# Kernel optimization log

Hardware: AMD Instinct MI355X
Metric: run time of the kernel (lower is better)

Reference implementation:

```python
import jax, jax.numpy as jnp
import numpy as np

B, S, D, H, E, K = 2, 2048, 1024, 4096, 8, 2


def setup_inputs() -> dict:
    key = jax.random.key(0)
    ks = jax.random.split(key, 7)
    sd = 1.0 / np.sqrt(D)
    sh = 1.0 / np.sqrt(H)
    return {
        "x": jax.random.normal(ks[0], (B, S, D), dtype=jnp.float32),
        "Wr": jax.random.uniform(ks[1], (D, E), jnp.float32, -sd, sd),
        "br": jnp.zeros((E,), jnp.float32),
        "W1": jax.random.uniform(ks[2], (E, D, H), jnp.float32, -sd, sd),
        "b1": jax.random.uniform(ks[3], (E, H), jnp.float32, -sd, sd),
        "W2": jax.random.uniform(ks[4], (E, H, D), jnp.float32, -sh, sh),
        "b2": jax.random.uniform(ks[5], (E, D), jnp.float32, -sh, sh),
    }


def reference(x, Wr, br, W1, b1, W2, b2):
    # Router
    router_logits = jnp.einsum("bsd,de->bse", x, Wr) + br          # [B,S,E]
    topk_logits, topk_idx = jax.lax.top_k(router_logits, K)          # [B,S,K]
    gates = jax.nn.softmax(topk_logits, axis=-1)                     # [B,S,K]

    # Dense all-expert FFN (math identical to masked per-expert GEMMs)
    h = jax.nn.gelu(jnp.einsum("bsd,edh->ebsh", x, W1) + b1[:, None, None, :],
                    approximate=False)                                # [E,B,S,H]
    y = jnp.einsum("ebsh,ehd->bsed", h, W2) + b2[None, None, :, :]    # [B,S,E,D]

    # Gather the top-k experts per token and combine with gates
    sel = jnp.take_along_axis(y, topk_idx[..., None], axis=2)         # [B,S,K,D]
    out = jnp.sum(gates[..., None] * sel, axis=2)                     # [B,S,D]

    # Load-balancing aux loss
    probs = jax.nn.softmax(router_logits, axis=-1)
    importance = probs.mean(axis=(0, 1))                              # [E]
    aux_loss = jnp.mean((importance - 1.0 / E) ** 2)
    return out, aux_loss
```

## Files before the change

### kernel.cpp

```cpp
#include <hip/hip_runtime.h>
#include <hip/hip_bf16.h>
#include <math.h>

#define NTOK 4096
#define DD   1024
#define HH   4096
#define EE   8
#define NSLOT 8192
#define NSLOT_PAD 8448
#define RBLK 128

typedef __bf16 bf16x8 __attribute__((ext_vector_type(8)));
typedef float  f32x4  __attribute__((ext_vector_type(4)));
typedef unsigned short u16x8 __attribute__((ext_vector_type(8)));

#define WAITCNT_VM(n) (((n) & 0xF) | (0x7 << 4) | (0xF << 8) | (((n) >> 4) << 14))

#define WS_COUNTS     0
#define WS_CURSORS    64
#define WS_OFFSETS    128
#define WS_IMP        256
#define WS_TOPK_IDX   512
#define WS_TOPK_GATE  33280
#define WS_SLOT_OF    66048
#define WS_TOKEN_LIST 98816
#define WS_XG         131584
#define WS_HBUF       17433088
#define WS_YBUF       86639104
#define WS_W1BT       120193536
#define WS_W2BT       187302400
#define WS_CNT_PART   (WS_HBUF + (size_t)NSLOT * HH * 2)
#define WS_IMP_PART   (WS_HBUF + (size_t)NSLOT * HH * 2 + 4096)

__device__ __forceinline__ float gelu_exact(float v) {
    return 0.5f * v * (1.0f + erff(v * 0.70710678118654752f));
}

__device__ __forceinline__ void async_copy16(const __bf16* g, __bf16* l) {
    __builtin_amdgcn_global_load_lds(
        (const __attribute__((address_space(1))) void*)g,
        (__attribute__((address_space(3))) void*)l, 16, 0, 0);
}

__launch_bounds__(256)
__global__ void router_kernel(const float* __restrict__ x,
                              const float* __restrict__ Wr,
                              const float* __restrict__ br,
                              int* __restrict__ cntPart,
                              float* __restrict__ impPart,
                              int* __restrict__ topk_idx,
                              float* __restrict__ topk_gate) {
    __shared__ float WrL[DD * EE];
    __shared__ float impW[4][EE];
    __shared__ int cntL[EE];
    int tid = threadIdx.x;
    int lane = tid & 63, wave = tid >> 6;
    int grp = lane >> 3, e = lane & 7;
    int t = blockIdx.x * 32 + wave * 8 + grp;

    for (int i = tid; i < DD * EE / 4; i += 256)
        ((float4*)WrL)[i] = ((const float4*)Wr)[i];
    if (tid < EE) cntL[tid] = 0;
    __syncthreads();

    const float* xr = x + (size_t)t * DD;
    float acc = 0.f;
#pragma unroll 4
    for (int d = 0; d < DD; d += 4) {
        float4 xv = *(const float4*)(xr + d);
        acc = fmaf(xv.x, WrL[(d + 0) * EE + e], acc);
        acc = fmaf(xv.y, WrL[(d + 1) * EE + e], acc);
        acc = fmaf(xv.z, WrL[(d + 2) * EE + e], acc);
        acc = fmaf(xv.w, WrL[(d + 3) * EE + e], acc);
    }
    float l = acc + br[e];

    float m = l;
#pragma unroll
    for (int mk = 1; mk <= 4; mk <<= 1) m = fmaxf(m, __shfl_xor(m, mk, 64));
    float p = expf(l - m);
    float s = p;
#pragma unroll
    for (int mk = 1; mk <= 4; mk <<= 1) s += __shfl_xor(s, mk, 64);
    p /= s;

    float bl = l; int be = e;
#pragma unroll
    for (int mk = 1; mk <= 4; mk <<= 1) {
        float ol = __shfl_xor(bl, mk, 64);
        int   oe = __shfl_xor(be, mk, 64);
        if (ol > bl || (ol == bl && oe < be)) { bl = ol; be = oe; }
    }
    int e1 = be; float l1 = bl;
    float cl = (e == e1) ? -INFINITY : l; int ce = e;
#pragma unroll
    for (int mk = 1; mk <= 4; mk <<= 1) {
        float ol = __shfl_xor(cl, mk, 64);
        int   oe = __shfl_xor(ce, mk, 64);
        if (ol > cl || (ol == cl && oe < ce)) { cl = ol; ce = oe; }
    }
    int e2 = ce; float l2 = cl;

    if (e == 0) {
        float bb = expf(l2 - l1);
        float g1 = 1.f / (1.f + bb);
        topk_idx[t * 2 + 0] = e1; topk_idx[t * 2 + 1] = e2;
        topk_gate[t * 2 + 0] = g1; topk_gate[t * 2 + 1] = bb * g1;
        atomicAdd(&cntL[e1], 1);
        atomicAdd(&cntL[e2], 1);
    }

#pragma unroll
    for (int mk = 8; mk <= 32; mk <<= 1) p += __shfl_xor(p, mk, 64);
    if (lane < 8) impW[wave][lane] = p;
    __syncthreads();
    if (tid < EE) {
        float v = impW[0][tid] + impW[1][tid] + impW[2][tid] + impW[3][tid];
        impPart[blockIdx.x * EE + tid] = v;
        cntPart[blockIdx.x * EE + tid] = cntL[tid];
    }
}

__launch_bounds__(256)
__global__ void scatter_kernel(const int* __restrict__ topk_idx,
                               const int* __restrict__ cntPart,
                               const float* __restrict__ impPart,
                               int* __restrict__ offsets,
                               int* __restrict__ token_list,
                               int* __restrict__ slot_of,
                               float* __restrict__ aux_out) {
    __shared__ int tot[EE], bef[EE], lcnt[EE];
    __shared__ float impS[EE];
    __shared__ int off[EE + 1];
    int tid = threadIdx.x, b = blockIdx.x;
    if (tid < EE) { tot[tid] = 0; bef[tid] = 0; lcnt[tid] = 0; impS[tid] = 0.f; }
    __syncthreads();
#pragma unroll
    for (int i = 0; i < 4; i++) {
        int idx = tid * 4 + i;
        int rb = idx >> 3, e = idx & 7;
        int c = cntPart[idx];
        atomicAdd(&tot[e], c);
        if (rb < b * 8) atomicAdd(&bef[e], c);
        if (b == 0) atomicAdd(&impS[e], impPart[idx]);
    }
    __syncthreads();
    if (tid == 0) {
        int o = 0;
        for (int e = 0; e < EE; e++) { off[e] = o; o += tot[e]; }
        off[EE] = o;
        if (b == 0) {
            for (int e = 0; e <= EE; e++) offsets[e] = off[e];
            float aux = 0.f;
            for (int e = 0; e < EE; e++) {
                float d = impS[e] / (float)NTOK - 1.0f / (float)EE;
                aux += d * d;
            }
            aux_out[0] = aux / (float)EE;
        }
    }
    __syncthreads();
    int t = b * 256 + tid;
    int e0 = topk_idx[t * 2 + 0], e1 = topk_idx[t * 2 + 1];
    int r0 = atomicAdd(&lcnt[e0], 1);
    int r1 = atomicAdd(&lcnt[e1], 1);
    int s0 = off[e0] + bef[e0] + r0;
    int s1 = off[e1] + bef[e1] + r1;
    token_list[s0] = t; token_list[s1] = t;
    slot_of[t * 2 + 0] = s0; slot_of[t * 2 + 1] = s1;
}

__launch_bounds__(256)
__global__ void gather_x_kernel(const float* __restrict__ x,
                                const int* __restrict__ token_list,
                                __bf16* __restrict__ xg) {
    int s = blockIdx.x;
    int t = token_list[s];
    int tid = threadIdx.x;
    float4 v = ((const float4*)(x + (size_t)t * DD))[tid];
    __bf16 tmp[4] __attribute__((aligned(8)));
    tmp[0] = (__bf16)v.x; tmp[1] = (__bf16)v.y;
    tmp[2] = (__bf16)v.z; tmp[3] = (__bf16)v.w;
    ((ushort4*)(xg + (size_t)s * DD))[tid] = *(ushort4*)tmp;
}

__launch_bounds__(256)
__global__ void transpose_w2_kernel(const float* __restrict__ W1,
                                    const float* __restrict__ W2,
                                    __bf16* __restrict__ W1bt,
                                    __bf16* __restrict__ W2bt) {
    int id = blockIdx.x;
    bool isw2 = id >= 8192;
    int rem = id & 8191;
    int e = rem >> 10, t = rem & 1023;
    const float* in; __bf16* out; int R, C, cx, ry;
    if (!isw2) { in = W1; out = W1bt; R = DD; C = HH; cx = t & 63; ry = t >> 6; }
    else       { in = W2; out = W2bt; R = HH; C = DD; cx = t & 15; ry = t >> 4; }
    int c0 = cx * 64, r0 = ry * 64;
    __shared__ float tile[64][65];
    int tid = threadIdx.x;
    const float* ip = in + (size_t)e * R * C;
#pragma unroll
    for (int i = 0; i < 4; i++) {
        int flat = i * 256 + tid;
        int r = flat >> 4, c4 = (flat & 15) * 4;
        float4 v = *(const float4*)(ip + (size_t)(r0 + r) * C + c0 + c4);
        tile[r][c4 + 0] = v.x; tile[r][c4 + 1] = v.y;
        tile[r][c4 + 2] = v.z; tile[r][c4 + 3] = v.w;
    }
    __syncthreads();
    __bf16* op = out + (size_t)e * C * R;
#pragma unroll
    for (int i = 0; i < 2; i++) {
        int flat = i * 256 + tid;
        int c = flat >> 3, r8 = (flat & 7) * 8;
        __bf16 tmp[8] __attribute__((aligned(16)));
#pragma unroll
        for (int j = 0; j < 8; j++) tmp[j] = (__bf16)tile[r8 + j][c];
        *(u16x8*)(op + (size_t)(c0 + c) * R + r0 + r8) = *(u16x8*)tmp;
    }
}

template <int N, int K, bool GELU, typename OutT>
__launch_bounds__(512, 4)
__global__ void gemm128_kernel(const __bf16* __restrict__ A,
                               const __bf16* __restrict__ Bt,
                               const float* __restrict__ bias,
                               const int* __restrict__ offsets,
                               OutT* __restrict__ Out) {
    constexpr int NT = K / 64;
    int e = blockIdx.z, ct = blockIdx.x, rt = blockIdx.y;
    int obase = offsets[e], cnt = offsets[e + 1] - obase;
    int m0 = rt * 128;
    if (m0 >= cnt) return;

    __shared__ __bf16 As[2][2][8 * 512];
    __shared__ __bf16 Bs[2][16 * 512];

    int tid = threadIdx.x, lane = tid & 63, wave = tid >> 6;
    int quad = lane >> 4, m16 = lane & 15;
    int wm = wave & 3, wn = wave >> 2;
    int srow = lane >> 3;
    int scol = ((lane & 7) ^ srow) * 8;

    const __bf16* Ag = A + (size_t)(obase + m0) * K + scol;
    const __bf16* Bg = Bt + ((size_t)e * N + (size_t)ct * 128) * K + scol;

    const __bf16* pA[2];
    const __bf16* pB[2];
#pragma unroll
    for (int h = 0; h < 2; h++) pA[h] = Ag + (size_t)(h * 64 + wave * 8 + srow) * K;
#pragma unroll
    for (int p = 0; p < 2; p++) pB[p] = Bg + (size_t)(p * 64 + wave * 8 + srow) * K;

    int swz = m16 & 7;
    int abase = (wm * 2 + (m16 >> 3)) * 512 + swz * 64;
    int bbase[4];
#pragma unroll
    for (int ni = 0; ni < 4; ni++)
        bbase[ni] = (ni * 4 + wn * 2 + (m16 >> 3)) * 512 + swz * 64;

    f32x4 acc[2][4] = {};
    bf16x8 af[2], bfr[4][2];

#define STG_A(buf, h, k0) async_copy16(pA[h] + (k0), &As[buf][h][wave * 512]);
#define STG_B(buf, k0)                                                        \
    { async_copy16(pB[0] + (k0), &Bs[buf][wave * 512]);                       \
      async_copy16(pB[1] + (k0), &Bs[buf][(wave + 8) * 512]); }

#define READ_A(buf, h)                                                        \
    { af[0] = *(const bf16x8*)(&As[buf][h][abase] + ((quad ^ swz) * 8));      \
      af[1] = *(const bf16x8*)(&As[buf][h][abase] + (((4 + quad) ^ swz) * 8)); }
#define READ_B(buf)                                                           \
    { _Pragma("unroll")                                                       \
      for (int ni = 0; ni < 4; ni++) {                                        \
          bfr[ni][0] = *(const bf16x8*)(&Bs[buf][bbase[ni]] + ((quad ^ swz) * 8)); \
          bfr[ni][1] = *(const bf16x8*)(&Bs[buf][bbase[ni]] + (((4 + quad) ^ swz) * 8)); } }

#define MMA(h)                                                                \
    { __builtin_amdgcn_s_setprio(1);                                         \
      _Pragma("unroll")                                                       \
      for (int kk = 0; kk < 2; kk++)                                          \
          _Pragma("unroll")                                                   \
          for (int ni = 0; ni < 4; ni++)                                      \
              acc[h][ni] = __builtin_amdgcn_mfma_f32_16x16x32_bf16(           \
                  af[kk], bfr[ni][kk], acc[h][ni], 0, 0, 0);                  \
      __builtin_amdgcn_s_setprio(0); }

    STG_A(0, 0, 0);
    STG_B(0, 0);
    STG_A(0, 1, 0);

    int cur = 0;
    for (int t = 0; t < NT - 1; t++) {
        int k1 = (t + 1) * 64, nxt = cur ^ 1;
        __builtin_amdgcn_s_waitcnt(WAITCNT_VM(1));
        __builtin_amdgcn_s_barrier();
        READ_A(cur, 0); READ_B(cur);
        STG_A(nxt, 0, k1); STG_B(nxt, k1);
        MMA(0);
        __builtin_amdgcn_s_waitcnt(WAITCNT_VM(3));
        __builtin_amdgcn_s_barrier();
        READ_A(cur, 1);
        STG_A(nxt, 1, k1);
        MMA(1);
        cur = nxt;
    }
    __builtin_amdgcn_s_waitcnt(WAITCNT_VM(1));
    __builtin_amdgcn_s_barrier();
    READ_A(cur, 0); READ_B(cur);
    MMA(0);
    __builtin_amdgcn_s_waitcnt(WAITCNT_VM(0));
    __builtin_amdgcn_s_barrier();
    READ_A(cur, 1);
    MMA(1);
#undef STG_A
#undef STG_B
#undef READ_A
#undef READ_B
#undef MMA

    float bv[4];
#pragma unroll
    for (int ni = 0; ni < 4; ni++)
        bv[ni] = bias[(size_t)e * N + ct * 128 + (ni * 2 + wn) * 16 + m16];
#pragma unroll
    for (int mi = 0; mi < 2; mi++) {
#pragma unroll
        for (int rr = 0; rr < 4; rr++) {
            int row = (mi * 4 + wm) * 16 + quad * 4 + rr;
            if (m0 + row < cnt) {
                size_t orow = (size_t)(obase + m0 + row) * N + (size_t)ct * 128;
#pragma unroll
                for (int ni = 0; ni < 4; ni++) {
                    float v = acc[mi][ni][rr] + bv[ni];
                    if (GELU) v = gelu_exact(v);
                    Out[orow + (ni * 2 + wn) * 16 + m16] = (OutT)v;
                }
            }
        }
    }
}

__launch_bounds__(256)
__global__ void combine_kernel(const float* __restrict__ ybuf,
                               const int* __restrict__ slot_of,
                               const float* __restrict__ topk_gate,
                               float* __restrict__ out) {
    int t = blockIdx.x;
    int tid = threadIdx.x;
    int s0 = slot_of[t * 2 + 0], s1 = slot_of[t * 2 + 1];
    float g0 = topk_gate[t * 2 + 0], g1 = topk_gate[t * 2 + 1];
    const float4* y0 = (const float4*)(ybuf + (size_t)s0 * DD);
    const float4* y1 = (const float4*)(ybuf + (size_t)s1 * DD);
    float4 a = y0[tid], b = y1[tid];
    float4 o;
    o.x = g0 * a.x + g1 * b.x;
    o.y = g0 * a.y + g1 * b.y;
    o.z = g0 * a.z + g1 * b.z;
    o.w = g0 * a.w + g1 * b.w;
    ((float4*)(out + (size_t)t * DD))[tid] = o;
}

extern "C" void kernel_launch(void* const* d_in, const int* in_sizes, int n_in,
                              void* d_out, int out_size, void* d_ws, size_t ws_size,
                              hipStream_t stream) {
    const float* x  = (const float*)d_in[0];
    const float* Wr = (const float*)d_in[1];
    const float* br = (const float*)d_in[2];
    const float* W1 = (const float*)d_in[3];
    const float* b1 = (const float*)d_in[4];
    const float* W2 = (const float*)d_in[5];
    const float* b2 = (const float*)d_in[6];
    float* out = (float*)d_out;

    char* ws = (char*)d_ws;
    int*    offsets    = (int*)(ws + WS_OFFSETS);
    int*    topk_idx   = (int*)(ws + WS_TOPK_IDX);
    float*  topk_gate  = (float*)(ws + WS_TOPK_GATE);
    int*    slot_of    = (int*)(ws + WS_SLOT_OF);
    int*    token_list = (int*)(ws + WS_TOKEN_LIST);
    __bf16* xg         = (__bf16*)(ws + WS_XG);
    __bf16* hbuf       = (__bf16*)(ws + WS_HBUF);
    float*  ybuf       = (float*)(ws + WS_YBUF);
    __bf16* W1bt       = (__bf16*)(ws + WS_W1BT);
    __bf16* W2bt       = (__bf16*)(ws + WS_W2BT);
    int*    cntPart    = (int*)(ws + WS_CNT_PART);
    float*  impPart    = (float*)(ws + WS_IMP_PART);

    router_kernel<<<RBLK, 256, 0, stream>>>(x, Wr, br, cntPart, impPart, topk_idx, topk_gate);
    scatter_kernel<<<NTOK / 256, 256, 0, stream>>>(topk_idx, cntPart, impPart,
                                                   offsets, token_list, slot_of,
                                                   out + (size_t)NTOK * DD);
    gather_x_kernel<<<NSLOT, 256, 0, stream>>>(x, token_list, xg);

    transpose_w2_kernel<<<16384, 256, 0, stream>>>(W1, W2, W1bt, W2bt);

    gemm128_kernel<HH, DD, true, __bf16>
        <<<dim3(HH / 128, 16, EE), 512, 0, stream>>>(xg, W1bt, b1, offsets, hbuf);
    gemm128_kernel<DD, HH, false, float>
        <<<dim3(DD / 128, 16, EE), 512, 0, stream>>>(hbuf, W2bt, b2, offsets, ybuf);

    combine_kernel<<<NTOK, 256, 0, stream>>>(ybuf, slot_of, topk_gate, out);
}
```

Measured before the change: 623.0 us.

## Rewrite router per-token-wave, scatter with shuffle reductions, and simplify GEMM tiling

The router now assigns one wave per token, reads Wr directly from global memory, and reduces the eight logits with wave shuffles across 1024 blocks instead of staging Wr in LDS. The scatter kernel replaces its shared-memory atomics with register accumulation and wave reductions. The double-buffered 512-thread GEMM is replaced by two single-buffered 256-thread kernels: a 128x128 tile with 4x4 MFMA per wave for the first GEMM and a 64x128 tile for the second, which doubles the grid to give more blocks. Removing the software pipelining cuts LDS use and complexity, but it exposes global-load latency at every K step.

```diff
diff --git a/kernel.cpp b/kernel.cpp
--- a/kernel.cpp
+++ b/kernel.cpp
@@ -8,13 +8,11 @@
 #define EE   8
 #define NSLOT 8192
 #define NSLOT_PAD 8448
-#define RBLK 128
+#define RBLK 1024
 
 typedef __bf16 bf16x8 __attribute__((ext_vector_type(8)));
 typedef float  f32x4  __attribute__((ext_vector_type(4)));
 typedef unsigned short u16x8 __attribute__((ext_vector_type(8)));
-
-#define WAITCNT_VM(n) (((n) & 0xF) | (0x7 << 4) | (0xF << 8) | (((n) >> 4) << 14))
 
 #define WS_COUNTS     0
 #define WS_CURSORS    64
@@ -30,7 +28,7 @@
 #define WS_W1BT       120193536
 #define WS_W2BT       187302400
 #define WS_CNT_PART   (WS_HBUF + (size_t)NSLOT * HH * 2)
-#define WS_IMP_PART   (WS_HBUF + (size_t)NSLOT * HH * 2 + 4096)
+#define WS_IMP_PART   (WS_HBUF + (size_t)NSLOT * HH * 2 + 32768)
 
 __device__ __forceinline__ float gelu_exact(float v) {
     return 0.5f * v * (1.0f + erff(v * 0.70710678118654752f));
@@ -50,74 +48,74 @@
                               float* __restrict__ impPart,
                               int* __restrict__ topk_idx,
                               float* __restrict__ topk_gate) {
-    __shared__ float WrL[DD * EE];
-    __shared__ float impW[4][EE];
     __shared__ int cntL[EE];
+    __shared__ float impL[EE];
     int tid = threadIdx.x;
     int lane = tid & 63, wave = tid >> 6;
-    int grp = lane >> 3, e = lane & 7;
-    int t = blockIdx.x * 32 + wave * 8 + grp;
-
-    for (int i = tid; i < DD * EE / 4; i += 256)
-        ((float4*)WrL)[i] = ((const float4*)Wr)[i];
-    if (tid < EE) cntL[tid] = 0;
+    int t = blockIdx.x * 4 + wave;
+
+    if (tid < EE) { cntL[tid] = 0; impL[tid] = 0.f; }
     __syncthreads();
 
-    const float* xr = x + (size_t)t * DD;
-    float acc = 0.f;
-#pragma unroll 4
-    for (int d = 0; d < DD; d += 4) {
-        float4 xv = *(const float4*)(xr + d);
-        acc = fmaf(xv.x, WrL[(d + 0) * EE + e], acc);
-        acc = fmaf(xv.y, WrL[(d + 1) * EE + e], acc);
-        acc = fmaf(xv.z, WrL[(d + 2) * EE + e], acc);
-        acc = fmaf(xv.w, WrL[(d + 3) * EE + e], acc);
-    }
-    float l = acc + br[e];
-
-    float m = l;
-#pragma unroll
-    for (int mk = 1; mk <= 4; mk <<= 1) m = fmaxf(m, __shfl_xor(m, mk, 64));
-    float p = expf(l - m);
-    float s = p;
-#pragma unroll
-    for (int mk = 1; mk <= 4; mk <<= 1) s += __shfl_xor(s, mk, 64);
-    p /= s;
-
-    float bl = l; int be = e;
-#pragma unroll
-    for (int mk = 1; mk <= 4; mk <<= 1) {
-        float ol = __shfl_xor(bl, mk, 64);
-        int   oe = __shfl_xor(be, mk, 64);
-        if (ol > bl || (ol == bl && oe < be)) { bl = ol; be = oe; }
-    }
-    int e1 = be; float l1 = bl;
-    float cl = (e == e1) ? -INFINITY : l; int ce = e;
-#pragma unroll
-    for (int mk = 1; mk <= 4; mk <<= 1) {
-        float ol = __shfl_xor(cl, mk, 64);
-        int   oe = __shfl_xor(ce, mk, 64);
-        if (ol > cl || (ol == cl && oe < ce)) { cl = ol; ce = oe; }
-    }
-    int e2 = ce; float l2 = cl;
-
-    if (e == 0) {
+    const float4* xp = (const float4*)(x + (size_t)t * DD + lane * 16);
+    float xs[16] __attribute__((aligned(16)));
+    *(float4*)&xs[0]  = xp[0];
+    *(float4*)&xs[4]  = xp[1];
+    *(float4*)&xs[8]  = xp[2];
+    *(float4*)&xs[12] = xp[3];
+
+    const float4* wp = (const float4*)(Wr + (size_t)lane * 16 * EE);
+    float a[8] = {0.f, 0.f, 0.f, 0.f, 0.f, 0.f, 0.f, 0.f};
+#pragma unroll
+    for (int j = 0; j < 16; j++) {
+        float4 w0 = wp[j * 2 + 0];
+        float4 w1 = wp[j * 2 + 1];
+        float xj = xs[j];
+        a[0] = fmaf(xj, w0.x, a[0]); a[1] = fmaf(xj, w0.y, a[1]);
+        a[2] = fmaf(xj, w0.z, a[2]); a[3] = fmaf(xj, w0.w, a[3]);
+        a[4] = fmaf(xj, w1.x, a[4]); a[5] = fmaf(xj, w1.y, a[5]);
+        a[6] = fmaf(xj, w1.z, a[6]); a[7] = fmaf(xj, w1.w, a[7]);
+    }
+#pragma unroll
+    for (int e = 0; e < 8; e++)
+#pragma unroll
+        for (int mk = 1; mk < 64; mk <<= 1)
+            a[e] += __shfl_xor(a[e], mk, 64);
+
+    float l[8];
+#pragma unroll
+    for (int e = 0; e < 8; e++) l[e] = a[e] + br[e];
+
+    float m = l[0];
+#pragma unroll
+    for (int e = 1; e < 8; e++) m = fmaxf(m, l[e]);
+    float p[8], s = 0.f;
+#pragma unroll
+    for (int e = 0; e < 8; e++) { p[e] = expf(l[e] - m); s += p[e]; }
+    float inv = 1.f / s;
+
+    int e1 = 0; float l1 = l[0];
+#pragma unroll
+    for (int e = 1; e < 8; e++) if (l[e] > l1) { l1 = l[e]; e1 = e; }
+    int e2 = -1; float l2 = -INFINITY;
+#pragma unroll
+    for (int e = 0; e < 8; e++)
+        if (e != e1 && l[e] > l2) { l2 = l[e]; e2 = e; }
+
+    if (lane == 0) {
         float bb = expf(l2 - l1);
         float g1 = 1.f / (1.f + bb);
         topk_idx[t * 2 + 0] = e1; topk_idx[t * 2 + 1] = e2;
         topk_gate[t * 2 + 0] = g1; topk_gate[t * 2 + 1] = bb * g1;
         atomicAdd(&cntL[e1], 1);
         atomicAdd(&cntL[e2], 1);
-    }
-
-#pragma unroll
-    for (int mk = 8; mk <= 32; mk <<= 1) p += __shfl_xor(p, mk, 64);
-    if (lane < 8) impW[wave][lane] = p;
+#pragma unroll
+        for (int e = 0; e < 8; e++) atomicAdd(&impL[e], p[e] * inv);
+    }
     __syncthreads();
     if (tid < EE) {
-        float v = impW[0][tid] + impW[1][tid] + impW[2][tid] + impW[3][tid];
-        impPart[blockIdx.x * EE + tid] = v;
         cntPart[blockIdx.x * EE + tid] = cntL[tid];
+        impPart[blockIdx.x * EE + tid] = impL[tid];
     }
 }
 
@@ -129,31 +127,63 @@
                                int* __restrict__ token_list,
                                int* __restrict__ slot_of,
                                float* __restrict__ aux_out) {
-    __shared__ int tot[EE], bef[EE], lcnt[EE];
-    __shared__ float impS[EE];
+    __shared__ int totW[4][EE], befW[4][EE];
+    __shared__ float impW[4][EE];
+    __shared__ int totS[EE], befS[EE], lcnt[EE];
     __shared__ int off[EE + 1];
     int tid = threadIdx.x, b = blockIdx.x;
-    if (tid < EE) { tot[tid] = 0; bef[tid] = 0; lcnt[tid] = 0; impS[tid] = 0.f; }
+    int lane = tid & 63, wave = tid >> 6;
+
+    int myTot[8] = {0,0,0,0,0,0,0,0};
+    int myBef[8] = {0,0,0,0,0,0,0,0};
+    float myImp[8] = {0.f,0.f,0.f,0.f,0.f,0.f,0.f,0.f};
+#pragma unroll
+    for (int i = 0; i < 4; i++) {
+        int rb = tid * 4 + i;
+        const int* row = cntPart + rb * 8;
+        const float* ir = impPart + rb * 8;
+        bool isbef = rb < b * 64;
+#pragma unroll
+        for (int e = 0; e < 8; e++) {
+            int c = row[e];
+            myTot[e] += c;
+            if (isbef) myBef[e] += c;
+            myImp[e] += ir[e];
+        }
+    }
+#pragma unroll
+    for (int e = 0; e < 8; e++)
+#pragma unroll
+        for (int mk = 1; mk < 64; mk <<= 1) {
+            myTot[e] += __shfl_xor(myTot[e], mk, 64);
+            myBef[e] += __shfl_xor(myBef[e], mk, 64);
+            myImp[e] += __shfl_xor(myImp[e], mk, 64);
+        }
+    if (lane == 0) {
+#pragma unroll
+        for (int e = 0; e < 8; e++) {
+            totW[wave][e] = myTot[e];
+            befW[wave][e] = myBef[e];
+            impW[wave][e] = myImp[e];
+        }
+    }
     __syncthreads();
-#pragma unroll
-    for (int i = 0; i < 4; i++) {
-        int idx = tid * 4 + i;
-        int rb = idx >> 3, e = idx & 7;
-        int c = cntPart[idx];
-        atomicAdd(&tot[e], c);
-        if (rb < b * 8) atomicAdd(&bef[e], c);
-        if (b == 0) atomicAdd(&impS[e], impPart[idx]);
+    if (tid < EE) {
+        totS[tid] = totW[0][tid] + totW[1][tid] + totW[2][tid] + totW[3][tid];
+        befS[tid] = befW[0][tid] + befW[1][tid] + befW[2][tid] + befW[3][tid];
+        lcnt[tid] = 0;
     }
     __syncthreads();
     if (tid == 0) {
         int o = 0;
-        for (int e = 0; e < EE; e++) { off[e] = o; o += tot[e]; }
+        for (int e = 0; e < EE; e++) { off[e] = o; o += totS[e]; }
         off[EE] = o;
         if (b == 0) {
             for (int e = 0; e <= EE; e++) offsets[e] = off[e];
             float aux = 0.f;
             for (int e = 0; e < EE; e++) {
-                float d = impS[e] / (float)NTOK - 1.0f / (float)EE;
+                float im = impW[0][e] + impW[1][e] + impW[2][e] + impW[3][e];
+                float d = im / (float)NTOK - 1.0f / (float)EE;
                 aux += d * d;
             }
             aux_out[0] = aux / (float)EE;
@@ -164,8 +194,8 @@
     int e0 = topk_idx[t * 2 + 0], e1 = topk_idx[t * 2 + 1];
     int r0 = atomicAdd(&lcnt[e0], 1);
     int r1 = atomicAdd(&lcnt[e1], 1);
-    int s0 = off[e0] + bef[e0] + r0;
-    int s1 = off[e1] + bef[e1] + r1;
+    int s0 = off[e0] + befS[e0] + r0;
+    int s1 = off[e1] + befS[e1] + r1;
     token_list[s0] = t; token_list[s1] = t;
     slot_of[t * 2 + 0] = s0; slot_of[t * 2 + 1] = s1;
 }
@@ -222,120 +252,186 @@
 }
 
 template <int N, int K, bool GELU, typename OutT>
-__launch_bounds__(512, 4)
-__global__ void gemm128_kernel(const __bf16* __restrict__ A,
-                               const __bf16* __restrict__ Bt,
-                               const float* __restrict__ bias,
-                               const int* __restrict__ offsets,
-                               OutT* __restrict__ Out) {
+__launch_bounds__(256, 4)
+__global__ void gemm97_kernel(const __bf16* __restrict__ A,
+                              const __bf16* __restrict__ Bt,
+                              const float* __restrict__ bias,
+                              const int* __restrict__ offsets,
+                              OutT* __restrict__ Out) {
     constexpr int NT = K / 64;
     int e = blockIdx.z, ct = blockIdx.x, rt = blockIdx.y;
     int obase = offsets[e], cnt = offsets[e + 1] - obase;
     int m0 = rt * 128;
     if (m0 >= cnt) return;
 
-    __shared__ __bf16 As[2][2][8 * 512];
-    __shared__ __bf16 Bs[2][16 * 512];
+    __shared__ __bf16 As[16 * 512];
+    __shared__ __bf16 Bs[16 * 512];
 
     int tid = threadIdx.x, lane = tid & 63, wave = tid >> 6;
     int quad = lane >> 4, m16 = lane & 15;
-    int wm = wave & 3, wn = wave >> 2;
+    int wm = wave & 1, wn = wave >> 1;
     int srow = lane >> 3;
     int scol = ((lane & 7) ^ srow) * 8;
 
     const __bf16* Ag = A + (size_t)(obase + m0) * K + scol;
     const __bf16* Bg = Bt + ((size_t)e * N + (size_t)ct * 128) * K + scol;
-
-    const __bf16* pA[2];
-    const __bf16* pB[2];
-#pragma unroll
-    for (int h = 0; h < 2; h++) pA[h] = Ag + (size_t)(h * 64 + wave * 8 + srow) * K;
-#pragma unroll
-    for (int p = 0; p < 2; p++) pB[p] = Bg + (size_t)(p * 64 + wave * 8 + srow) * K;
-
-    int swz = m16 & 7;
-    int abase = (wm * 2 + (m16 >> 3)) * 512 + swz * 64;
-    int bbase[4];
+    const __bf16* pA[4];
+    const __bf16* pB[4];
+#pragma unroll
+    for (int r = 0; r < 4; r++) {
+        pA[r] = Ag + (size_t)((r * 4 + wave) * 8 + srow) * K;
+        pB[r] = Bg + (size_t)((r * 4 + wave) * 8 + srow) * K;
+    }
+
+    f32x4 acc[4][4] = {};
+
+    for (int kt = 0; kt < NT; kt++) {
+        int k0 = kt * 64;
+        __syncthreads();
+#pragma unroll
+        for (int r = 0; r < 4; r++)
+            async_copy16(pA[r] + k0, &As[(r * 4 + wave) * 512]);
+#pragma unroll
+        for (int r = 0; r < 4; r++)
+            async_copy16(pB[r] + k0, &Bs[(r * 4 + wave) * 512]);
+        __syncthreads();
+        __builtin_amdgcn_s_setprio(1);
+#pragma unroll
+        for (int ks = 0; ks < 2; ks++) {
+            bf16x8 af[4], bf[4];
+#pragma unroll
+            for (int mi = 0; mi < 4; mi++) {
+                int r = wm * 64 + mi * 16 + m16;
+                af[mi] = *(const bf16x8*)(&As[(r >> 3) * 512 + (r & 7) * 64
+                                          + (((ks * 4 + quad) ^ (r & 7)) * 8)]);
+            }
+#pragma unroll
+            for (int ni = 0; ni < 4; ni++) {
+                int r = wn * 64 + ni * 16 + m16;
+                bf[ni] = *(const bf16x8*)(&Bs[(r >> 3) * 512 + (r & 7) * 64
+                                          + (((ks * 4 + quad) ^ (r & 7)) * 8)]);
+            }
+#pragma unroll
+            for (int mi = 0; mi < 4; mi++)
+#pragma unroll
+                for (int ni = 0; ni < 4; ni++)
+                    acc[mi][ni] = __builtin_amdgcn_mfma_f32_16x16x32_bf16(
+                        af[mi], bf[ni], acc[mi][ni], 0, 0, 0);
+        }
+        __builtin_amdgcn_s_setprio(0);
+    }
+
+    float bv[4];
 #pragma unroll
     for (int ni = 0; ni < 4; ni++)
-        bbase[ni] = (ni * 4 + wn * 2 + (m16 >> 3)) * 512 + swz * 64;
-
-    f32x4 acc[2][4] = {};
-    bf16x8 af[2], bfr[4][2];
-
-#define STG_A(buf, h, k0) async_copy16(pA[h] + (k0), &As[buf][h][wave * 512]);
-#define STG_B(buf, k0)                                                        \
-    { async_copy16(pB[0] + (k0), &Bs[buf][wave * 512]);                       \
-      async_copy16(pB[1] + (k0), &Bs[buf][(wave + 8) * 512]); }
-
-#define READ_A(buf, h)                                                        \
-    { af[0] = *(const bf16x8*)(&As[buf][h][abase] + ((quad ^ swz) * 8));      \
-      af[1] = *(const bf16x8*)(&As[buf][h][abase] + (((4 + quad) ^ swz) * 8)); }
-#define READ_B(buf)                                                           \
-    { _Pragma("unroll")                                                       \
-      for (int ni = 0; ni < 4; ni++) {                                        \
-          bfr[ni][0] = *(const bf16x8*)(&Bs[buf][bbase[ni]] + ((quad ^ swz) * 8)); \
-          bfr[ni][1] = *(const bf16x8*)(&Bs[buf][bbase[ni]] + (((4 + quad) ^ swz) * 8)); } }
-
-#define MMA(h)                                                                \
-    { __builtin_amdgcn_s_setprio(1);                                         \
-      _Pragma("unroll")                                                       \
-      for (int kk = 0; kk < 2; kk++)                                          \
-          _Pragma("unroll")                                                   \
-          for (int ni = 0; ni < 4; ni++)                                      \
-              acc[h][ni] = __builtin_amdgcn_mfma_f32_16x16x32_bf16(           \
-                  af[kk], bfr[ni][kk], acc[h][ni], 0, 0, 0);                  \
-      __builtin_amdgcn_s_setprio(0); }
-
-    STG_A(0, 0, 0);
-    STG_B(0, 0);
-    STG_A(0, 1, 0);
-
-    int cur = 0;
-    for (int t = 0; t < NT - 1; t++) {
-        int k1 = (t + 1) * 64, nxt = cur ^ 1;
-        __builtin_amdgcn_s_waitcnt(WAITCNT_VM(1));
-        __builtin_amdgcn_s_barrier();
-        READ_A(cur, 0); READ_B(cur);
-        STG_A(nxt, 0, k1); STG_B(nxt, k1);
-        MMA(0);
-        __builtin_amdgcn_s_waitcnt(WAITCNT_VM(3));
-        __builtin_amdgcn_s_barrier();
-        READ_A(cur, 1);
-        STG_A(nxt, 1, k1);
-        MMA(1);
-        cur = nxt;
-    }
-    __builtin_amdgcn_s_waitcnt(WAITCNT_VM(1));
-    __builtin_amdgcn_s_barrier();
-    READ_A(cur, 0); READ_B(cur);
-    MMA(0);
-    __builtin_amdgcn_s_waitcnt(WAITCNT_VM(0));
-    __builtin_amdgcn_s_barrier();
-    READ_A(cur, 1);
-    MMA(1);
-#undef STG_A
-#undef STG_B
-#undef READ_A
-#undef READ_B
-#undef MMA
-
-    float bv[4];
-#pragma unroll
-    for (int ni = 0; ni < 4; ni++)
-        bv[ni] = bias[(size_t)e * N + ct * 128 + (ni * 2 + wn) * 16 + m16];
-#pragma unroll
-    for (int mi = 0; mi < 2; mi++) {
+        bv[ni] = bias[(size_t)e * N + ct * 128 + wn * 64 + ni * 16 + m16];
+#pragma unroll
+    for (int mi = 0; mi < 4; mi++) {
 #pragma unroll
         for (int rr = 0; rr < 4; rr++) {
-            int row = (mi * 4 + wm) * 16 + quad * 4 + rr;
+            int row = wm * 64 + mi * 16 + quad * 4 + rr;
             if (m0 + row < cnt) {
-                size_t orow = (size_t)(obase + m0 + row) * N + (size_t)ct * 128;
+                size_t orow = (size_t)(obase + m0 + row) * N
+                              + (size_t)ct * 128 + wn * 64;
 #pragma unroll
                 for (int ni = 0; ni < 4; ni++) {
                     float v = acc[mi][ni][rr] + bv[ni];
                     if (GELU) v = gelu_exact(v);
-                    Out[orow + (ni * 2 + wn) * 16 + m16] = (OutT)v;
+                    Out[orow + ni * 16 + m16] = (OutT)v;
+                }
+            }
+        }
+    }
+}
+
+template <int N, int K, bool GELU, typename OutT>
+__launch_bounds__(256, 4)
+__global__ void gemm64_kernel(const __bf16* __restrict__ A,
+                              const __bf16* __restrict__ Bt,
+                              const float* __restrict__ bias,
+                              const int* __restrict__ offsets,
+                              OutT* __restrict__ Out) {
+    constexpr int NT = K / 64;
+    int e = blockIdx.z, ct = blockIdx.x, rt = blockIdx.y;
+    int obase = offsets[e], cnt = offsets[e + 1] - obase;
+    int m0 = rt * 64;
+    if (m0 >= cnt) return;
+
+    __shared__ __bf16 As[8 * 512];
+    __shared__ __bf16 Bs[16 * 512];
+
+    int tid = threadIdx.x, lane = tid & 63, wave = tid >> 6;
+    int quad = lane >> 4, m16 = lane & 15;
+    int wn = wave;
+    int srow = lane >> 3;
+    int scol = ((lane & 7) ^ srow) * 8;
+
+    const __bf16* Ag = A + (size_t)(obase + m0) * K + scol;
+    const __bf16* Bg = Bt + ((size_t)e * N + (size_t)ct * 128) * K + scol;
+    const __bf16* pA[2];
+    const __bf16* pB[4];
+#pragma unroll
+    for (int r = 0; r < 2; r++)
+        pA[r] = Ag + (size_t)((r * 4 + wave) * 8 + srow) * K;
+#pragma unroll
+    for (int r = 0; r < 4; r++)
+        pB[r] = Bg + (size_t)((r * 4 + wave) * 8 + srow) * K;
+
+    f32x4 acc[4][2] = {};
+
+    for (int kt = 0; kt < NT; kt++) {
+        int k0 = kt * 64;
+        __syncthreads();
+#pragma unroll
+        for (int r = 0; r < 2; r++)
+            async_copy16(pA[r] + k0, &As[(r * 4 + wave) * 512]);
+#pragma unroll
+        for (int r = 0; r < 4; r++)
+            async_copy16(pB[r] + k0, &Bs[(r * 4 + wave) * 512]);
+        __syncthreads();
+        __builtin_amdgcn_s_setprio(1);
+#pragma unroll
+        for (int ks = 0; ks < 2; ks++) {
+            bf16x8 af[4], bf[2];
+#pragma unroll
+            for (int mi = 0; mi < 4; mi++) {
+                int r = mi * 16 + m16;
+                af[mi] = *(const bf16x8*)(&As[(r >> 3) * 512 + (r & 7) * 64
+                                          + (((ks * 4 + quad) ^ (r & 7)) * 8)]);
+            }
+#pragma unroll
+            for (int ni = 0; ni < 2; ni++) {
+                int r = wn * 32 + ni * 16 + m16;
+                bf[ni] = *(const bf16x8*)(&Bs[(r >> 3) * 512 + (r & 7) * 64
+                                          + (((ks * 4 + quad) ^ (r & 7)) * 8)]);
+            }
+#pragma unroll
+            for (int mi = 0; mi < 4; mi++)
+#pragma unroll
+                for (int ni = 0; ni < 2; ni++)
+                    acc[mi][ni] = __builtin_amdgcn_mfma_f32_16x16x32_bf16(
+                        af[mi], bf[ni], acc[mi][ni], 0, 0, 0);
+        }
+        __builtin_amdgcn_s_setprio(0);
+    }
+
+    float bv[2];
+#pragma unroll
+    for (int ni = 0; ni < 2; ni++)
+        bv[ni] = bias[(size_t)e * N + ct * 128 + wn * 32 + ni * 16 + m16];
+#pragma unroll
+    for (int mi = 0; mi < 4; mi++) {
+#pragma unroll
+        for (int rr = 0; rr < 4; rr++) {
+            int row = mi * 16 + quad * 4 + rr;
+            if (m0 + row < cnt) {
+                size_t orow = (size_t)(obase + m0 + row) * N
+                              + (size_t)ct * 128 + wn * 32;
+#pragma unroll
+                for (int ni = 0; ni < 2; ni++) {
+                    float v = acc[mi][ni][rr] + bv[ni];
+                    if (GELU) v = gelu_exact(v);
+                    Out[orow + ni * 16 + m16] = (OutT)v;
                 }
             }
         }
@@ -396,10 +492,10 @@
 
     transpose_w2_kernel<<<16384, 256, 0, stream>>>(W1, W2, W1bt, W2bt);
 
-    gemm128_kernel<HH, DD, true, __bf16>
-        <<<dim3(HH / 128, 16, EE), 512, 0, stream>>>(xg, W1bt, b1, offsets, hbuf);
-    gemm128_kernel<DD, HH, false, float>
-        <<<dim3(DD / 128, 16, EE), 512, 0, stream>>>(hbuf, W2bt, b2, offsets, ybuf);
+    gemm97_kernel<HH, DD, true, __bf16>
+        <<<dim3(HH / 128, 16, EE), 256, 0, stream>>>(xg, W1bt, b1, offsets, hbuf);
+    gemm64_kernel<DD, HH, false, float>
+        <<<dim3(DD / 128, 32, EE), 256, 0, stream>>>(hbuf, W2bt, b2, offsets, ybuf);
 
     combine_kernel<<<NTOK, 256, 0, stream>>>(ybuf, slot_of, topk_gate, out);
 }
```

Result: faster. 610.7 us (-2.0%).
